# Optimization experiments

Measured on AMD Instinct MI355X. Metric: run time of the kernel, lower is better.

The kernel has to match this reference:

```python
import jax, jax.numpy as jnp
import numpy as np

B, S, E = 8, 2048, 512
H = 8          # attention heads (and also number of sampling points)
P = 8          # deformable sampling points per token
Dh = E // H


def setup_inputs() -> dict:
    key = jax.random.key(0)
    ks = jax.random.split(key, 9)
    scale = 0.02
    return {
        "q": jax.random.normal(ks[0], (B, S, E), jnp.float32),
        "k": jax.random.normal(ks[1], (B, S, E), jnp.float32),
        "v": jax.random.normal(ks[2], (B, S, E), jnp.float32),
        "offset_w": jax.random.normal(ks[3], (2 * P, E), jnp.float32) * scale,
        "offset_b": jnp.zeros((2 * P,), jnp.float32),
        "in_proj_w": jax.random.normal(ks[4], (3 * E, E), jnp.float32) * scale,
        "in_proj_b": jnp.zeros((3 * E,), jnp.float32),
        "out_w": jax.random.normal(ks[5], (E, E), jnp.float32) * scale,
        "out_b": jnp.zeros((E,), jnp.float32),
    }


def reference(q, k, v, offset_w, offset_b, in_proj_w, in_proj_b, out_w, out_b):
    b, s, e = q.shape
    # learned offsets: [B,S,P,2]; only component 0 is used as a temporal offset
    offsets = (q @ offset_w.T + offset_b).reshape(b, s, P, 2)
    t = jnp.arange(s, dtype=q.dtype)[None, :, None]                # [1,S,1]
    # index = clamp(int(t + off0), 0, S-1); python int() truncates toward zero
    idx = jnp.clip(jnp.trunc(t + offsets[..., 0]).astype(jnp.int32), 0, s - 1)  # [B,S,P]
    # gather sampled K/V: [B,S,P,E]
    sk = jnp.take_along_axis(k[:, :, None, :], idx[..., None], axis=1)
    sv = jnp.take_along_axis(v[:, :, None, :], idx[..., None], axis=1)

    # nn.MultiheadAttention with query len 1 per token, kv len P, batch = B*S
    wq, wk, wv = in_proj_w[:e], in_proj_w[e:2 * e], in_proj_w[2 * e:]
    bq, bk, bv = in_proj_b[:e], in_proj_b[e:2 * e], in_proj_b[2 * e:]
    n = b * s
    qp = (q.reshape(n, e) @ wq.T + bq).reshape(n, H, Dh)            # [N,H,Dh]
    kp = (sk.reshape(n, P, e) @ wk.T + bk).reshape(n, P, H, Dh)     # [N,P,H,Dh]
    vp = (sv.reshape(n, P, e) @ wv.T + bv).reshape(n, P, H, Dh)
    scores = jnp.einsum('nhd,nphd->nhp', qp, kp) / np.sqrt(Dh)      # [N,H,P]
    attn = jax.nn.softmax(scores, axis=-1)
    ctx = jnp.einsum('nhp,nphd->nhd', attn, vp).reshape(n, e)       # [N,E]
    out = ctx @ out_w.T + out_b
    return out.reshape(b, s, e)
```

## Files before the change

kernel.cpp:

```cpp
#include <hip/hip_runtime.h>

#define S_LEN 2048
#define E_DIM 512
#define NTOK  16384

typedef __bf16 bf16x8_t __attribute__((ext_vector_type(8)));
typedef float f32x4_t __attribute__((ext_vector_type(4)));
typedef unsigned short u16x8_t __attribute__((ext_vector_type(8)));

__device__ __forceinline__ float bf2f(unsigned short h) {
  return __uint_as_float(((unsigned)h) << 16);
}
__device__ __forceinline__ u16x8_t cvt8n(float4 a, float4 b) {
  bf16x8_t t;
  t[0] = (__bf16)a.x; t[1] = (__bf16)a.y; t[2] = (__bf16)a.z; t[3] = (__bf16)a.w;
  t[4] = (__bf16)b.x; t[5] = (__bf16)b.y; t[6] = (__bf16)b.z; t[7] = (__bf16)b.w;
  union { bf16x8_t h; u16x8_t u; } cv; cv.h = t; return cv.u;
}
__device__ __forceinline__ void gload16(const void* g, void* l) {
  __builtin_amdgcn_global_load_lds(
      (const __attribute__((address_space(1))) unsigned int*)g,
      (__attribute__((address_space(3))) unsigned int*)l, 16, 0, 0);
}

__global__ __launch_bounds__(256)
void prepass_kernel(const float* __restrict__ q, const float* __restrict__ k,
                    const float* __restrict__ v, const float* __restrict__ ipw,
                    const float* __restrict__ outw, const float* __restrict__ ow,
                    const float* __restrict__ ob, int* __restrict__ idx,
                    unsigned short* __restrict__ Qbf, unsigned short* __restrict__ Kb,
                    unsigned short* __restrict__ Vb, unsigned short* __restrict__ Wb,
                    unsigned short* __restrict__ OWb)
{
  const int bid = blockIdx.x;
  if (bid >= 4096) {
    const float* src; unsigned short* dst; size_t off;
    if (bid < 8192)       { src = k;    dst = Kb;  off = (size_t)(bid - 4096) * 2048; }
    else if (bid < 12288) { src = v;    dst = Vb;  off = (size_t)(bid - 8192) * 2048; }
    else if (bid < 12672) { src = ipw;  dst = Wb;  off = (size_t)(bid - 12288) * 2048; }
    else                  { src = outw; dst = OWb; off = (size_t)(bid - 12672) * 2048; }
    const size_t i = off + (size_t)threadIdx.x * 8;
    const float4 a = *(const float4*)(src + i);
    const float4 b = *(const float4*)(src + i + 4);
    *(u16x8_t*)(dst + i) = cvt8n(a, b);
    return;
  }
  const int wid  = threadIdx.x >> 6;
  const int lane = threadIdx.x & 63;
  const int n = bid * 4 + wid;
  const int s = n & (S_LEN - 1);
  const float* qr = q + (size_t)n * E_DIM + lane * 8;
  const float4 q0 = *(const float4*)qr;
  const float4 q1 = *(const float4*)(qr + 4);
  *(u16x8_t*)(Qbf + (size_t)n * E_DIM + lane * 8) = cvt8n(q0, q1);
  float myoff = 0.f;
  #pragma unroll
  for (int p = 0; p < 8; ++p) {
    const float* wr = ow + (size_t)(2 * p) * E_DIM + lane * 8;
    const float4 w0 = *(const float4*)wr;
    const float4 w1 = *(const float4*)(wr + 4);
    float acc = q0.x*w0.x + q0.y*w0.y + q0.z*w0.z + q0.w*w0.w
              + q1.x*w1.x + q1.y*w1.y + q1.z*w1.z + q1.w*w1.w;
    #pragma unroll
    for (int d = 32; d; d >>= 1) acc += __shfl_xor(acc, d, 64);
    if ((lane & 7) == p) myoff = acc;
  }
  if (lane < 8) {
    float off = myoff + ob[2 * lane];
    float val = (float)s + off;
    int id = (int)truncf(val);
    id = id < 0 ? 0 : (id > S_LEN - 1 ? S_LEN - 1 : id);
    idx[n * 8 + lane] = id;
  }
}

template<int OUT_BF16>
__global__ __launch_bounds__(256, 2)
void gemm_kernel(const unsigned short* __restrict__ A0, const unsigned short* __restrict__ A1,
                 const unsigned short* __restrict__ A2, const unsigned short* __restrict__ W,
                 const float* __restrict__ bias, void* __restrict__ Cout)
{
  __shared__ __align__(16) unsigned short sA[4][128 * 32];
  __shared__ __align__(16) unsigned short sB[4][128 * 32];

  const int z = blockIdx.z;
  const unsigned short* A = (z == 0) ? A0 : ((z == 1) ? A1 : A2);
  const unsigned short* Wz = W + (size_t)z * E_DIM * E_DIM;
  const float* bz = bias + (size_t)z * E_DIM;

  const int t    = threadIdx.x;
  const int lane = t & 63;
  const int wid  = t >> 6;
  const int wm   = wid >> 1;
  const int wn   = wid & 1;
  const size_t m0 = (size_t)blockIdx.x * 128;
  const size_t n0 = (size_t)blockIdx.y * 128;

  const int srow   = wid * 32 + (lane >> 2);
  const int schunk = (lane & 3) ^ ((lane >> 3) & 3);
  const unsigned short* gA = A  + (m0 + srow) * E_DIM + schunk * 8;
  const unsigned short* gB = Wz + (n0 + srow) * E_DIM + schunk * 8;

#define STAGE(slot, t_) do { \
    gload16(gA + (t_) * 32,              &sA[slot][(wid * 32) * 32]); \
    gload16(gA + (t_) * 32 + 16 * E_DIM, &sA[slot][(wid * 32 + 16) * 32]); \
    gload16(gB + (t_) * 32,              &sB[slot][(wid * 32) * 32]); \
    gload16(gB + (t_) * 32 + 16 * E_DIM, &sB[slot][(wid * 32 + 16) * 32]); \
  } while (0)

  f32x4_t acc[4][4];
  #pragma unroll
  for (int i = 0; i < 4; ++i)
    #pragma unroll
    for (int j = 0; j < 4; ++j)
      acc[i][j] = (f32x4_t){0.f, 0.f, 0.f, 0.f};

  STAGE(0, 0); STAGE(1, 1); STAGE(2, 2);

  const int fr    = lane & 15;
  const int cswz8 = (((lane >> 4) ^ ((fr >> 1) & 3)) << 3);

  #pragma unroll
  for (int tt = 0; tt < 16; ++tt) {
    if (tt + 3 < 16) STAGE((tt + 3) & 3, tt + 3);
    if (tt < 13)       asm volatile("s_waitcnt vmcnt(12)" ::: "memory");
    else if (tt == 13) asm volatile("s_waitcnt vmcnt(8)"  ::: "memory");
    else if (tt == 14) asm volatile("s_waitcnt vmcnt(4)"  ::: "memory");
    else               asm volatile("s_waitcnt vmcnt(0)"  ::: "memory");
    __builtin_amdgcn_sched_barrier(0);
    __builtin_amdgcn_s_barrier();
    __builtin_amdgcn_sched_barrier(0);
    const int sl = tt & 3;
    bf16x8_t af[4], bfv[4];
    #pragma unroll
    for (int i = 0; i < 4; ++i)
      af[i] = *(const bf16x8_t*)&sA[sl][(wm * 64 + i * 16 + fr) * 32 + cswz8];
    #pragma unroll
    for (int j = 0; j < 4; ++j)
      bfv[j] = *(const bf16x8_t*)&sB[sl][(wn * 64 + j * 16 + fr) * 32 + cswz8];
    __builtin_amdgcn_s_setprio(1);
    #pragma unroll
    for (int i = 0; i < 4; ++i)
      #pragma unroll
      for (int j = 0; j < 4; ++j)
        acc[i][j] = __builtin_amdgcn_mfma_f32_16x16x32_bf16(af[i], bfv[j], acc[i][j], 0, 0, 0);
    __builtin_amdgcn_s_setprio(0);
    __builtin_amdgcn_sched_barrier(0);
    __builtin_amdgcn_s_barrier();
    __builtin_amdgcn_sched_barrier(0);
  }
#undef STAGE

  unsigned short* Cb = (unsigned short*)Cout + (size_t)z * NTOK * E_DIM;
  float* Cf = (float*)Cout;
  #pragma unroll
  for (int i = 0; i < 4; ++i) {
    const int row = (int)m0 + wm * 64 + i * 16 + (lane >> 4) * 4;
    #pragma unroll
    for (int j = 0; j < 4; ++j) {
      const int col = (int)n0 + wn * 64 + j * 16 + fr;
      const float bv = bz[col];
      #pragma unroll
      for (int r = 0; r < 4; ++r) {
        const float val = acc[i][j][r] + bv;
        if constexpr (OUT_BF16)
          Cb[(size_t)(row + r) * E_DIM + col] = __builtin_bit_cast(unsigned short, (__bf16)val);
        else
          Cf[(size_t)(row + r) * E_DIM + col] = val;
      }
    }
  }
}

__global__ __launch_bounds__(256)
void attn_kernel(const unsigned short* __restrict__ Qp, const unsigned short* __restrict__ Kp,
                 const unsigned short* __restrict__ Vp, const int* __restrict__ idx,
                 unsigned short* __restrict__ ctx)
{
  const int wid  = threadIdx.x >> 6;
  const int lane = threadIdx.x & 63;
  const int n = blockIdx.x * 4 + wid;
  const int b = n >> 11;
  const int h = lane >> 3;
  const int p = lane & 7;

  const int id = idx[n * 8 + p];
  const size_t krow = ((size_t)(b << 11) + id) * E_DIM + h * 64;
  const unsigned short* qb = Qp + (size_t)n * E_DIM + h * 64;

  float sc = 0.f;
  #pragma unroll
  for (int j = 0; j < 8; ++j) {
    u16x8_t qv = *(const u16x8_t*)(qb + j * 8);
    u16x8_t kv = *(const u16x8_t*)(Kp + krow + j * 8);
    #pragma unroll
    for (int e = 0; e < 8; ++e) sc += bf2f(qv[e]) * bf2f(kv[e]);
  }
  sc *= 0.125f;

  float m = sc;
  m = fmaxf(m, __shfl_xor(m, 1, 64));
  m = fmaxf(m, __shfl_xor(m, 2, 64));
  m = fmaxf(m, __shfl_xor(m, 4, 64));
  const float ex = __expf(sc - m);
  float dsum = ex;
  dsum += __shfl_xor(dsum, 1, 64);
  dsum += __shfl_xor(dsum, 2, 64);
  dsum += __shfl_xor(dsum, 4, 64);
  const float attn = ex / dsum;

  const int d0 = p * 8;
  float cacc[8];
  #pragma unroll
  for (int j = 0; j < 8; ++j) cacc[j] = 0.f;
  #pragma unroll
  for (int pp = 0; pp < 8; ++pp) {
    const float ap = __shfl(attn, (lane & 56) + pp, 64);
    const int  idp = __shfl(id,   (lane & 56) + pp, 64);
    const unsigned short* vb = Vp + ((size_t)(b << 11) + idp) * E_DIM + h * 64 + d0;
    u16x8_t vv = *(const u16x8_t*)vb;
    #pragma unroll
    for (int j = 0; j < 8; ++j) cacc[j] += ap * bf2f(vv[j]);
  }
  u16x8_t cc;
  #pragma unroll
  for (int j = 0; j < 8; ++j) cc[j] = __builtin_bit_cast(unsigned short, (__bf16)cacc[j]);
  *(u16x8_t*)(ctx + (size_t)n * E_DIM + h * 64 + d0) = cc;
}

extern "C" void kernel_launch(void* const* d_in, const int* in_sizes, int n_in,
                              void* d_out, int out_size, void* d_ws, size_t ws_size,
                              hipStream_t stream) {
  const float* q        = (const float*)d_in[0];
  const float* k        = (const float*)d_in[1];
  const float* v        = (const float*)d_in[2];
  const float* offset_w = (const float*)d_in[3];
  const float* offset_b = (const float*)d_in[4];
  const float* in_proj_w = (const float*)d_in[5];
  const float* in_proj_b = (const float*)d_in[6];
  const float* out_w    = (const float*)d_in[7];
  const float* out_b    = (const float*)d_in[8];

  char* ws = (char*)d_ws;
  unsigned short* Qbf = (unsigned short*)ws;
  unsigned short* Kbf = Qbf + (size_t)NTOK * E_DIM;
  unsigned short* Vbf = Kbf + (size_t)NTOK * E_DIM;
  unsigned short* Wb  = Vbf + (size_t)NTOK * E_DIM;
  unsigned short* OWb = Wb + (size_t)3 * E_DIM * E_DIM;
  unsigned short* Qp  = OWb + (size_t)E_DIM * E_DIM;
  unsigned short* Kp  = Qp + (size_t)NTOK * E_DIM;
  unsigned short* Vp  = Kp + (size_t)NTOK * E_DIM;
  int* idxb = (int*)(Vp + (size_t)NTOK * E_DIM);
  unsigned short* ctxb = Qbf;

  prepass_kernel<<<12800, 256, 0, stream>>>(q, k, v, in_proj_w, out_w, offset_w, offset_b,
                                            idxb, Qbf, Kbf, Vbf, Wb, OWb);
  gemm_kernel<1><<<dim3(NTOK / 128, E_DIM / 128, 3), 256, 0, stream>>>(
      Qbf, Kbf, Vbf, Wb, in_proj_b, (void*)Qp);
  attn_kernel<<<NTOK / 4, 256, 0, stream>>>(Qp, Kp, Vp, idxb, ctxb);
  gemm_kernel<0><<<dim3(NTOK / 128, E_DIM / 128, 1), 256, 0, stream>>>(
      ctxb, ctxb, ctxb, OWb, out_b, d_out);
}
```

Before: 109.4 us.

## Replace 128x128 GEMM with 256x256 eight-wave tile and split-phase double buffering

The projection GEMMs move from a 128x128 tile with 4 waves and a 4-stage K=32 pipeline to a 256x256 tile with 8 waves, K=64 steps and double-buffered LDS. Each wave computes a 128x64 sub-tile in quadrants, with LDS reads and global prefetch interleaved around MFMA phases. The aim is more data reuse per loaded byte and less barrier overhead per MFMA. In exchange it uses 128KB of LDS per block, which limits occupancy, and launches far fewer blocks (e.g. 64x2 for the output GEMM), which may underfill the CUs.

```diff
diff --git a/kernel.cpp b/kernel.cpp
--- a/kernel.cpp
+++ b/kernel.cpp
@@ -74,96 +74,128 @@
   }
 }
 
-template<int OUT_BF16>
-__global__ __launch_bounds__(256, 2)
-void gemm_kernel(const unsigned short* __restrict__ A0, const unsigned short* __restrict__ A1,
-                 const unsigned short* __restrict__ A2, const unsigned short* __restrict__ W,
-                 const float* __restrict__ bias, void* __restrict__ Cout)
+template<int OUT_MODE>
+__global__ __launch_bounds__(512, 2)
+void gemm8_kernel(const unsigned short* __restrict__ A0, const unsigned short* __restrict__ A1,
+                  const unsigned short* __restrict__ A2, const unsigned short* __restrict__ W,
+                  const float* __restrict__ bias, void* __restrict__ Cout)
 {
-  __shared__ __align__(16) unsigned short sA[4][128 * 32];
-  __shared__ __align__(16) unsigned short sB[4][128 * 32];
+  __shared__ __align__(16) unsigned short sA[2][256 * 64];
+  __shared__ __align__(16) unsigned short sB[2][256 * 64];
 
   const int z = blockIdx.z;
-  const unsigned short* A = (z == 0) ? A0 : ((z == 1) ? A1 : A2);
+  const unsigned short* A  = (z == 0) ? A0 : ((z == 1) ? A1 : A2);
   const unsigned short* Wz = W + (size_t)z * E_DIM * E_DIM;
-  const float* bz = bias + (size_t)z * E_DIM;
 
   const int t    = threadIdx.x;
   const int lane = t & 63;
   const int wid  = t >> 6;
-  const int wm   = wid >> 1;
-  const int wn   = wid & 1;
-  const size_t m0 = (size_t)blockIdx.x * 128;
-  const size_t n0 = (size_t)blockIdx.y * 128;
-
-  const int srow   = wid * 32 + (lane >> 2);
-  const int schunk = (lane & 3) ^ ((lane >> 3) & 3);
-  const unsigned short* gA = A  + (m0 + srow) * E_DIM + schunk * 8;
-  const unsigned short* gB = Wz + (n0 + srow) * E_DIM + schunk * 8;
-
-#define STAGE(slot, t_) do { \
-    gload16(gA + (t_) * 32,              &sA[slot][(wid * 32) * 32]); \
-    gload16(gA + (t_) * 32 + 16 * E_DIM, &sA[slot][(wid * 32 + 16) * 32]); \
-    gload16(gB + (t_) * 32,              &sB[slot][(wid * 32) * 32]); \
-    gload16(gB + (t_) * 32 + 16 * E_DIM, &sB[slot][(wid * 32 + 16) * 32]); \
+  const int wm   = wid >> 2;
+  const int wn   = wid & 3;
+  const size_t m0 = (size_t)blockIdx.x * 256;
+  const size_t n0 = (size_t)blockIdx.y * 256;
+
+  const unsigned short* gA = A  + (m0 + wid * 16 + (lane >> 3)) * E_DIM + (((lane & 7) ^ (lane >> 3)) << 3);
+  const unsigned short* gB = Wz + (n0 + wid * 16 + (lane >> 3)) * E_DIM + (((lane & 7) ^ (lane >> 3)) << 3);
+
+#define STG_A(slot, kt, h) do { \
+    gload16(gA + (size_t)((h) * 128) * E_DIM + (kt) * 64,     &sA[slot][((h) * 128 + wid * 16) * 64]); \
+    gload16(gA + (size_t)((h) * 128 + 8) * E_DIM + (kt) * 64, &sA[slot][((h) * 128 + wid * 16 + 8) * 64]); \
   } while (0)
-
-  f32x4_t acc[4][4];
-  #pragma unroll
-  for (int i = 0; i < 4; ++i)
+#define STG_B(slot, kt, h) do { \
+    gload16(gB + (size_t)((h) * 128) * E_DIM + (kt) * 64,     &sB[slot][((h) * 128 + wid * 16) * 64]); \
+    gload16(gB + (size_t)((h) * 128 + 8) * E_DIM + (kt) * 64, &sB[slot][((h) * 128 + wid * 16 + 8) * 64]); \
+  } while (0)
+
+  f32x4_t acc[8][4];
+  #pragma unroll
+  for (int i = 0; i < 8; ++i)
     #pragma unroll
     for (int j = 0; j < 4; ++j)
       acc[i][j] = (f32x4_t){0.f, 0.f, 0.f, 0.f};
 
-  STAGE(0, 0); STAGE(1, 1); STAGE(2, 2);
-
-  const int fr    = lane & 15;
-  const int cswz8 = (((lane >> 4) ^ ((fr >> 1) & 3)) << 3);
-
-  #pragma unroll
-  for (int tt = 0; tt < 16; ++tt) {
-    if (tt + 3 < 16) STAGE((tt + 3) & 3, tt + 3);
-    if (tt < 13)       asm volatile("s_waitcnt vmcnt(12)" ::: "memory");
-    else if (tt == 13) asm volatile("s_waitcnt vmcnt(8)"  ::: "memory");
-    else if (tt == 14) asm volatile("s_waitcnt vmcnt(4)"  ::: "memory");
-    else               asm volatile("s_waitcnt vmcnt(0)"  ::: "memory");
-    __builtin_amdgcn_sched_barrier(0);
-    __builtin_amdgcn_s_barrier();
-    __builtin_amdgcn_sched_barrier(0);
-    const int sl = tt & 3;
-    bf16x8_t af[4], bfv[4];
-    #pragma unroll
-    for (int i = 0; i < 4; ++i)
-      af[i] = *(const bf16x8_t*)&sA[sl][(wm * 64 + i * 16 + fr) * 32 + cswz8];
-    #pragma unroll
-    for (int j = 0; j < 4; ++j)
-      bfv[j] = *(const bf16x8_t*)&sB[sl][(wn * 64 + j * 16 + fr) * 32 + cswz8];
+  bf16x8_t af[4][2], bf0[2][2], bf1[2][2];
+  const int fr = lane & 15;
+  const int rx = fr & 7;
+  const int kc = lane >> 4;
+
+#define RD_A(sl, msub) do { _Pragma("unroll") for (int i_ = 0; i_ < 4; ++i_) { \
+    const int row = wm * 128 + ((msub) * 4 + i_) * 16 + fr; \
+    af[i_][0] = *(const bf16x8_t*)&sA[sl][row * 64 + ((kc ^ rx) << 3)]; \
+    af[i_][1] = *(const bf16x8_t*)&sA[sl][row * 64 + (((4 + kc) ^ rx) << 3)]; \
+  } } while (0)
+#define RD_B(sl, dst, nsub) do { _Pragma("unroll") for (int j_ = 0; j_ < 2; ++j_) { \
+    const int row = wn * 64 + ((nsub) * 2 + j_) * 16 + fr; \
+    dst[j_][0] = *(const bf16x8_t*)&sB[sl][row * 64 + ((kc ^ rx) << 3)]; \
+    dst[j_][1] = *(const bf16x8_t*)&sB[sl][row * 64 + (((4 + kc) ^ rx) << 3)]; \
+  } } while (0)
+#define MFMA_Q(ms, ns, bb) do { _Pragma("unroll") for (int i_ = 0; i_ < 4; ++i_) \
+    _Pragma("unroll") for (int j_ = 0; j_ < 2; ++j_) { \
+      acc[(ms)*4+i_][(ns)*2+j_] = __builtin_amdgcn_mfma_f32_16x16x32_bf16(af[i_][0], bb[j_][0], acc[(ms)*4+i_][(ns)*2+j_], 0, 0, 0); \
+      acc[(ms)*4+i_][(ns)*2+j_] = __builtin_amdgcn_mfma_f32_16x16x32_bf16(af[i_][1], bb[j_][1], acc[(ms)*4+i_][(ns)*2+j_], 0, 0, 0); \
+  } } while (0)
+
+  STG_A(0, 0, 0); STG_B(0, 0, 0); STG_A(0, 0, 1); STG_B(0, 0, 1);
+  asm volatile("s_waitcnt vmcnt(0)" ::: "memory");
+  __builtin_amdgcn_sched_barrier(0);
+  __builtin_amdgcn_s_barrier();
+
+  for (int kt = 0; kt < 8; ++kt) {
+    const int sl = kt & 1;
+    RD_A(sl, 0); RD_B(sl, bf0, 0);
+    if (kt < 7) { STG_A(sl ^ 1, kt + 1, 0); STG_B(sl ^ 1, kt + 1, 0); }
+    __builtin_amdgcn_s_barrier();
+    asm volatile("s_waitcnt lgkmcnt(0)" ::: "memory");
+    __builtin_amdgcn_sched_barrier(0);
     __builtin_amdgcn_s_setprio(1);
-    #pragma unroll
-    for (int i = 0; i < 4; ++i)
-      #pragma unroll
-      for (int j = 0; j < 4; ++j)
-        acc[i][j] = __builtin_amdgcn_mfma_f32_16x16x32_bf16(af[i], bfv[j], acc[i][j], 0, 0, 0);
+    MFMA_Q(0, 0, bf0);
     __builtin_amdgcn_s_setprio(0);
     __builtin_amdgcn_sched_barrier(0);
     __builtin_amdgcn_s_barrier();
-    __builtin_amdgcn_sched_barrier(0);
-  }
-#undef STAGE
+    RD_B(sl, bf1, 1);
+    if (kt < 7) { STG_A(sl ^ 1, kt + 1, 1); STG_B(sl ^ 1, kt + 1, 1); }
+    __builtin_amdgcn_s_barrier();
+    asm volatile("s_waitcnt lgkmcnt(0)" ::: "memory");
+    __builtin_amdgcn_sched_barrier(0);
+    __builtin_amdgcn_s_setprio(1);
+    MFMA_Q(0, 1, bf1);
+    __builtin_amdgcn_s_setprio(0);
+    __builtin_amdgcn_sched_barrier(0);
+    __builtin_amdgcn_s_barrier();
+    RD_A(sl, 1);
+    __builtin_amdgcn_s_barrier();
+    asm volatile("s_waitcnt lgkmcnt(0)" ::: "memory");
+    __builtin_amdgcn_sched_barrier(0);
+    __builtin_amdgcn_s_setprio(1);
+    MFMA_Q(1, 0, bf0);
+    MFMA_Q(1, 1, bf1);
+    __builtin_amdgcn_s_setprio(0);
+    __builtin_amdgcn_sched_barrier(0);
+    if (kt < 7) {
+      asm volatile("s_waitcnt vmcnt(0)" ::: "memory");
+      __builtin_amdgcn_sched_barrier(0);
+      __builtin_amdgcn_s_barrier();
+    }
+  }
+#undef STG_A
+#undef STG_B
+#undef RD_A
+#undef RD_B
+#undef MFMA_Q
 
   unsigned short* Cb = (unsigned short*)Cout + (size_t)z * NTOK * E_DIM;
   float* Cf = (float*)Cout;
   #pragma unroll
-  for (int i = 0; i < 4; ++i) {
-    const int row = (int)m0 + wm * 64 + i * 16 + (lane >> 4) * 4;
-    #pragma unroll
-    for (int j = 0; j < 4; ++j) {
-      const int col = (int)n0 + wn * 64 + j * 16 + fr;
-      const float bv = bz[col];
+  for (int mi = 0; mi < 8; ++mi) {
+    const int row = (int)m0 + wm * 128 + mi * 16 + (lane >> 4) * 4;
+    #pragma unroll
+    for (int nj = 0; nj < 4; ++nj) {
+      const int col = (int)n0 + wn * 64 + nj * 16 + fr;
+      const float bv = bias[z * E_DIM + col];
       #pragma unroll
       for (int r = 0; r < 4; ++r) {
-        const float val = acc[i][j][r] + bv;
-        if constexpr (OUT_BF16)
+        const float val = acc[mi][nj][r] + bv;
+        if constexpr (OUT_MODE)
           Cb[(size_t)(row + r) * E_DIM + col] = __builtin_bit_cast(unsigned short, (__bf16)val);
         else
           Cf[(size_t)(row + r) * E_DIM + col] = val;
@@ -255,9 +287,9 @@
 
   prepass_kernel<<<12800, 256, 0, stream>>>(q, k, v, in_proj_w, out_w, offset_w, offset_b,
                                             idxb, Qbf, Kbf, Vbf, Wb, OWb);
-  gemm_kernel<1><<<dim3(NTOK / 128, E_DIM / 128, 3), 256, 0, stream>>>(
+  gemm8_kernel<1><<<dim3(NTOK / 256, E_DIM / 256, 3), 512, 0, stream>>>(
       Qbf, Kbf, Vbf, Wb, in_proj_b, (void*)Qp);
   attn_kernel<<<NTOK / 4, 256, 0, stream>>>(Qp, Kp, Vp, idxb, ctxb);
-  gemm_kernel<0><<<dim3(NTOK / 128, E_DIM / 128, 1), 256, 0, stream>>>(
+  gemm8_kernel<0><<<dim3(NTOK / 256, E_DIM / 256, 1), 512, 0, stream>>>(
       ctxb, ctxb, ctxb, OWb, out_b, d_out);
 }
```

After: 112.5 us. +2.8%, slower.
